# Kernel tuning notes

Measured on AMD Instinct MI355X. Metric: run time of the kernel, lower is better.

## Reference

```python
import jax, jax.numpy as jnp
import numpy as np

N, E = 50000, 800000
IN, H, OUT = 500, 128, 64


def _gcn_layer(x, src, dst, norm, W, b):
    # Linear transform first (PyG GCNConv applies lin before propagate)
    h = x @ W                                   # [N, F_out]
    msg = norm[:, None] * h[src]                # [E', F_out] gather
    out = jax.ops.segment_sum(msg, dst, num_segments=N)  # scatter-add
    return out + b


def setup_inputs() -> dict:
    key = jax.random.key(0)
    k = jax.random.split(key, 6)
    x = jax.random.normal(k[0], (N, IN), jnp.float32)
    edge_index = jax.random.randint(k[1], (2, E), 0, N, dtype=jnp.int32)
    # Glorot-style init like PyG GCNConv
    W1 = jax.random.normal(k[2], (IN, H), jnp.float32) * (1.0 / np.sqrt(IN))
    b1 = jnp.zeros((H,), jnp.float32)
    W2 = jax.random.normal(k[3], (H, OUT), jnp.float32) * (1.0 / np.sqrt(H))
    b2 = jnp.zeros((OUT,), jnp.float32)
    return {"x": x, "edge_index": edge_index, "W1": W1, "b1": b1, "W2": W2, "b2": b2}


def reference(x, edge_index, W1, b1, W2, b2):
    # Add self loops (PyG GCNConv default add_self_loops=True)
    loops = jnp.arange(N, dtype=edge_index.dtype)
    src = jnp.concatenate([edge_index[0], loops])
    dst = jnp.concatenate([edge_index[1], loops])
    # Symmetric degree normalization: deg computed on targets (col)
    deg = jax.ops.segment_sum(jnp.ones_like(src, dtype=x.dtype), dst, num_segments=N)
    dis = jnp.where(deg > 0, jax.lax.rsqrt(jnp.maximum(deg, 1.0)), 0.0)
    norm = dis[src] * dis[dst]                  # [E+N]
    h = jax.nn.relu(_gcn_layer(x, src, dst, norm, W1, b1))
    return _gcn_layer(h, src, dst, norm, W2, b2)
```

## Files before the change

kernel.cpp:

```cpp
#include <hip/hip_runtime.h>
#include <hip/hip_bf16.h>


typedef __attribute__((ext_vector_type(4))) float f32x4;
typedef __attribute__((ext_vector_type(8))) short short8;

static __device__ __forceinline__ unsigned short f2bf(float f) {
    unsigned int u = __float_as_uint(f);
    u += 0x7FFF + ((u >> 16) & 1);
    return (unsigned short)(u >> 16);
}
static __device__ __forceinline__ float bf2f(unsigned short h) {
    return __uint_as_float(((unsigned int)h) << 16);
}

static __device__ __forceinline__ void glds16(const void* g, void* l) {
    __builtin_amdgcn_global_load_lds(
        (const __attribute__((address_space(1))) void*)g,
        (__attribute__((address_space(3))) void*)l, 16, 0, 0);
}

__global__ void prep_deg(const float* __restrict__ W1, const float* __restrict__ W2,
                         unsigned short* __restrict__ I1, unsigned short* __restrict__ I2,
                         const int* __restrict__ dst, int* __restrict__ deg, int E) {
    const int bid = blockIdx.x;
    if (bid < 72) {
        int idx = bid * 256 + threadIdx.x;
        const int total1 = 16 * 1024;
        if (idx < total1) {
            int kt = idx >> 10, pl = (idx >> 9) & 1, slot = (idx >> 7) & 3, col = idx & 127;
            int k0 = kt * 32 + slot * 8;
#pragma unroll
            for (int j = 0; j < 8; j++) {
                int k = k0 + j;
                float v = (k < 500) ? W1[(size_t)k * 128 + col] : 0.f;
                unsigned short h = f2bf(v);
                I1[(size_t)idx * 8 + j] = pl ? f2bf(v - bf2f(h)) : h;
            }
        } else {
            int i2 = idx - total1;
            if (i2 < 2048) {
                int kt = i2 >> 9, pl = (i2 >> 8) & 1, slot = (i2 >> 6) & 3, col = i2 & 63;
                int k0 = kt * 32 + slot * 8;
#pragma unroll
                for (int j = 0; j < 8; j++) {
                    float v = W2[(size_t)(k0 + j) * 64 + col];
                    unsigned short h = f2bf(v);
                    I2[(size_t)i2 * 8 + j] = pl ? f2bf(v - bf2f(h)) : h;
                }
            }
        }
    } else {
        int e = (bid - 72) * 256 + threadIdx.x;
        if (e < E) atomicAdd(&deg[dst[e]], 1);
    }
}

__global__ void scan_part(const int* __restrict__ deg, int* __restrict__ bsum, int N) {
    int tid = threadIdx.x, lane = tid & 63, wid = tid >> 6;
    int i = blockIdx.x * 256 + tid;
    int v = (i < N) ? deg[i] : 0;
#pragma unroll
    for (int off = 1; off < 64; off <<= 1) v += __shfl_xor(v, off, 64);
    __shared__ int ws[4];
    if (lane == 0) ws[wid] = v;
    __syncthreads();
    if (tid == 0) bsum[blockIdx.x] = ws[0] + ws[1] + ws[2] + ws[3];
}

__global__ __launch_bounds__(1024) void scan_top(const int* __restrict__ bsum, int nb,
                                                 int* __restrict__ boff, int* __restrict__ rp, int N) {
    __shared__ int wsum[16];
    int tid = threadIdx.x, lane = tid & 63, wid = tid >> 6;
    int v = (tid < nb) ? bsum[tid] : 0;
    int x = v;
#pragma unroll
    for (int off = 1; off < 64; off <<= 1) {
        int t = __shfl_up(x, off, 64);
        if (lane >= off) x += t;
    }
    if (lane == 63) wsum[wid] = x;
    __syncthreads();
    if (tid < 16) {
        int y = wsum[tid];
#pragma unroll
        for (int off = 1; off < 16; off <<= 1) {
            int t = __shfl_up(y, off, 16);
            if (tid >= off) y += t;
        }
        wsum[tid] = y;
    }
    __syncthreads();
    int base = wid ? wsum[wid - 1] : 0;
    if (tid < nb) boff[tid] = base + x - v;
    if (tid == 0) rp[N] = wsum[15];
}

__global__ void scan_final(int* __restrict__ deg, const int* __restrict__ boff,
                           int* __restrict__ rp, int* __restrict__ cursor, int N) {
    int tid = threadIdx.x, lane = tid & 63, wid = tid >> 6;
    int i = blockIdx.x * 256 + tid;
    int v = (i < N) ? deg[i] : 0;
    int x = v;
#pragma unroll
    for (int off = 1; off < 64; off <<= 1) {
        int t = __shfl_up(x, off, 64);
        if (lane >= off) x += t;
    }
    __shared__ int wsum[4];
    if (lane == 63) wsum[wid] = x;
    __syncthreads();
    int base = boff[blockIdx.x];
    for (int ww = 0; ww < wid; ww++) base += wsum[ww];
    int ex = base + x - v;
    if (i < N) {
        rp[i] = ex;
        cursor[i] = ex;
        ((float*)deg)[i] = rsqrtf((float)(v + 1));
    }
}

template<int BN, int KT, int KFULL, bool ABF16>
__device__ __forceinline__ void gemm_body(
    int bid, unsigned char* sm,
    const void* __restrict__ Av, const unsigned char* __restrict__ Wimg,
    unsigned short* __restrict__ C, int M, int K) {
    constexpr int AELT = ABF16 ? 2 : 4;
    constexpr int ABYTES = 64 * 32 * AELT;
    constexpr int BBYTES = BN * 128;
    constexpr int STEP = ABYTES + BBYTES;
    constexpr int AINST = ABYTES / 1024;
    constexpr int BINST = BBYTES / 1024;
    constexpr int IPW = (AINST + BINST) / 4;
    constexpr int BIPW = BINST / 4;
    constexpr int NF = BN / 16;
    constexpr int AKC = 16 / AELT;

    const int tid = threadIdx.x, lane = tid & 63, w = tid >> 6;
    const int lrow = lane & 15, lq = lane >> 4;
    const int bm = bid * 64;

    f32x4 acc[NF] = {};

    float pr[8];
    if constexpr (!ABF16 && KFULL < KT) {
        const float* A = (const float*)Av;
        const int prow = tid >> 2, pk = (tid & 3) * 8;
        const int grow = bm + prow;
#pragma unroll
        for (int j = 0; j < 8; j++) {
            int k = KFULL * 32 + pk + j;
            pr[j] = (grow < M && k < K) ? A[(size_t)grow * K + k] : 0.f;
        }
    }

    auto STAGE = [&](int kt, int buf) {
        unsigned char* base = sm + buf * STEP;
#pragma unroll
        for (int j = 0; j < IPW; j++) {
            int g = w * IPW + j;
            if (g < AINST) {
                int srow = bm + lane; if (srow >= M) srow = M - 1;
                if constexpr (ABF16)
                    glds16((const unsigned short*)Av + (size_t)srow * K + kt * 32 + g * AKC,
                           base + g * 1024);
                else
                    glds16((const float*)Av + (size_t)srow * K + kt * 32 + g * AKC,
                           base + g * 1024);
            } else {
                int b = g - AINST;
                glds16(Wimg + (size_t)kt * BBYTES + (size_t)b * 1024 + lane * 16,
                       base + ABYTES + b * 1024);
            }
        }
    };
    auto STAGE_B = [&](int kt, int buf) {
        unsigned char* base = sm + buf * STEP;
#pragma unroll
        for (int j = 0; j < BIPW; j++) {
            int b = w * BIPW + j;
            glds16(Wimg + (size_t)kt * BBYTES + (size_t)b * 1024 + lane * 16,
                   base + ABYTES + b * 1024);
        }
    };
    auto REGWRITE = [&](int buf) {
        if constexpr (!ABF16) {
            const int prow = tid >> 2, pk = (tid & 3) * 8;
            unsigned char* base = sm + buf * STEP;
            int s0 = pk >> 2;
            *(float4*)(base + s0 * 1024 + prow * 16) = make_float4(pr[0], pr[1], pr[2], pr[3]);
            *(float4*)(base + (s0 + 1) * 1024 + prow * 16) = make_float4(pr[4], pr[5], pr[6], pr[7]);
        }
    };
    auto COMPUTE = [&](int buf) {
        const unsigned char* base = sm + buf * STEP;
        short8 ah, al;
        if constexpr (ABF16) {
            int r = w * 16 + lrow;
            ah = *(const short8*)(base + lq * 1024 + r * 16);
        } else {
            int r = w * 16 + lrow;
            float4 f0 = *(const float4*)(base + (lq * 2) * 1024 + r * 16);
            float4 f1 = *(const float4*)(base + (lq * 2 + 1) * 1024 + r * 16);
            float fv[8] = {f0.x, f0.y, f0.z, f0.w, f1.x, f1.y, f1.z, f1.w};
#pragma unroll
            for (int e = 0; e < 8; e++) {
                unsigned short hu = f2bf(fv[e]);
                ah[e] = (short)hu;
                al[e] = (short)f2bf(fv[e] - bf2f(hu));
            }
        }
        short8 bh[NF], bl[NF];
#pragma unroll
        for (int n = 0; n < NF; n++) {
            int c = n * 16 + lrow;
            bh[n] = *(const short8*)(base + ABYTES + lq * (BN * 16) + c * 16);
            bl[n] = *(const short8*)(base + ABYTES + BBYTES / 2 + lq * (BN * 16) + c * 16);
        }
#pragma unroll
        for (int n = 0; n < NF; n++) {
            acc[n] = __builtin_amdgcn_mfma_f32_16x16x32_bf16(ah, bh[n], acc[n], 0, 0, 0);
            if constexpr (!ABF16)
                acc[n] = __builtin_amdgcn_mfma_f32_16x16x32_bf16(al, bh[n], acc[n], 0, 0, 0);
            acc[n] = __builtin_amdgcn_mfma_f32_16x16x32_bf16(ah, bl[n], acc[n], 0, 0, 0);
        }
    };

    STAGE(0, 0);
    __syncthreads();
    int cur = 0;
    for (int kt = 0; kt < KT; kt++) {
        if (kt + 1 < KT) {
            if constexpr (!ABF16 && KFULL < KT) {
                if (kt + 1 == KFULL) { STAGE_B(kt + 1, cur ^ 1); REGWRITE(cur ^ 1); }
                else STAGE(kt + 1, cur ^ 1);
            } else {
                STAGE(kt + 1, cur ^ 1);
            }
        }
        COMPUTE(cur);
        __syncthreads();
        cur ^= 1;
    }

#pragma unroll
    for (int n = 0; n < NF; n++)
#pragma unroll
        for (int q = 0; q < 4; q++) {
            int row = bm + w * 16 + (lane >> 4) * 4 + q;
            int col = n * 16 + (lane & 15);
            if (row < M) C[(size_t)row * BN + col] = f2bf(acc[n][q]);
        }
}

template<int BN, int KT>
__global__ __launch_bounds__(256) void gemm_glds_bf(
    const unsigned short* __restrict__ A, const unsigned char* __restrict__ Wimg,
    unsigned short* __restrict__ C, int M, int K) {
    __shared__ unsigned char sm[2 * (4096 + BN * 128)];
    gemm_body<BN, KT, KT, true>(blockIdx.x, sm, A, Wimg, C, M, K);
}

template<int BN, int KT, int KFULL>
__global__ __launch_bounds__(256) void fat_gemm_csr(
    const float* __restrict__ A, const unsigned char* __restrict__ Wimg,
    unsigned short* __restrict__ C, int M, int K,
    const int* __restrict__ src, const int* __restrict__ dst,
    int* __restrict__ cursor, int* __restrict__ csr_src, int E,
    int ngemm, int ncsr) {
    __shared__ unsigned char sm[2 * (8192 + BN * 128)];
    const int bid = blockIdx.x;
    const int stripe = bid / 5, pos = bid % 5;
    if (pos == 0) {
        if (stripe < ngemm)
            gemm_body<BN, KT, KFULL, false>(stripe, sm, A, Wimg, C, M, K);
    } else {
        int c = stripe * 4 + pos - 1;
        if (c < ncsr) {
            int e = c * 256 + threadIdx.x;
            if (e < E) {
                int p = atomicAdd(&cursor[dst[e]], 1);
                csr_src[p] = src[e];
            }
        }
    }
}

__global__ __launch_bounds__(256) void gather128(
    const int* __restrict__ rp, const int* __restrict__ csr,
    const float* __restrict__ dis, const unsigned short* __restrict__ h,
    const float* __restrict__ bias, unsigned short* __restrict__ out, int Nn) {
    int n = (blockIdx.x * 256 + threadIdx.x) >> 6;
    int lane = threadIdx.x & 63;
    if (n >= Nn) return;
    const int hh = lane >> 5;
    const int l = lane & 31;
    int beg = rp[n], end = rp[n + 1];
    float4 a0 = {0,0,0,0}, a1 = {0,0,0,0}, a2 = {0,0,0,0}, a3 = {0,0,0,0};
    auto P = [&](int e, float4& a) {
        int s = csr[e];
        float w = dis[s];
        ushort4 v = *(const ushort4*)&h[(size_t)s * 128 + l * 4];
        a.x = fmaf(w, bf2f(v.x), a.x); a.y = fmaf(w, bf2f(v.y), a.y);
        a.z = fmaf(w, bf2f(v.z), a.z); a.w = fmaf(w, bf2f(v.w), a.w);
    };
    int j = beg + hh;
    for (; j + 6 < end; j += 8) { P(j, a0); P(j + 2, a1); P(j + 4, a2); P(j + 6, a3); }
    for (; j < end; j += 2) P(j, a0);
    float4 acc;
    acc.x = (a0.x + a1.x) + (a2.x + a3.x);
    acc.y = (a0.y + a1.y) + (a2.y + a3.y);
    acc.z = (a0.z + a1.z) + (a2.z + a3.z);
    acc.w = (a0.w + a1.w) + (a2.w + a3.w);
    acc.x += __shfl_xor(acc.x, 32);
    acc.y += __shfl_xor(acc.y, 32);
    acc.z += __shfl_xor(acc.z, 32);
    acc.w += __shfl_xor(acc.w, 32);
    float dn = dis[n];
    ushort4 hv = *(const ushort4*)&h[(size_t)n * 128 + l * 4];
    float4 b4 = *(const float4*)&bias[l * 4];
    if (hh == 0) {
        ushort4 o;
        o.x = f2bf(fmaxf(dn * (acc.x + dn * bf2f(hv.x)) + b4.x, 0.f));
        o.y = f2bf(fmaxf(dn * (acc.y + dn * bf2f(hv.y)) + b4.y, 0.f));
        o.z = f2bf(fmaxf(dn * (acc.z + dn * bf2f(hv.z)) + b4.z, 0.f));
        o.w = f2bf(fmaxf(dn * (acc.w + dn * bf2f(hv.w)) + b4.w, 0.f));
        *(ushort4*)&out[(size_t)n * 128 + l * 4] = o;
    }
}

__global__ __launch_bounds__(256) void gather64(
    const int* __restrict__ rp, const int* __restrict__ csr,
    const float* __restrict__ dis, const unsigned short* __restrict__ h,
    const float* __restrict__ bias, float* __restrict__ out, int Nn) {
    int n = (blockIdx.x * 256 + threadIdx.x) >> 6;
    int lane = threadIdx.x & 63;
    if (n >= Nn) return;
    const int q = lane >> 4;
    const int l = lane & 15;
    int beg = rp[n], end = rp[n + 1];
    float4 a0 = {0,0,0,0}, a1 = {0,0,0,0};
    auto P = [&](int e, float4& a) {
        int s = csr[e];
        float w = dis[s];
        ushort4 v = *(const ushort4*)&h[(size_t)s * 64 + l * 4];
        a.x = fmaf(w, bf2f(v.x), a.x); a.y = fmaf(w, bf2f(v.y), a.y);
        a.z = fmaf(w, bf2f(v.z), a.z); a.w = fmaf(w, bf2f(v.w), a.w);
    };
    int j = beg + q;
    for (; j + 4 < end; j += 8) { P(j, a0); P(j + 4, a1); }
    for (; j < end; j += 4) P(j, a0);
    float4 acc;
    acc.x = a0.x + a1.x; acc.y = a0.y + a1.y;
    acc.z = a0.z + a1.z; acc.w = a0.w + a1.w;
    acc.x += __shfl_xor(acc.x, 16); acc.x += __shfl_xor(acc.x, 32);
    acc.y += __shfl_xor(acc.y, 16); acc.y += __shfl_xor(acc.y, 32);
    acc.z += __shfl_xor(acc.z, 16); acc.z += __shfl_xor(acc.z, 32);
    acc.w += __shfl_xor(acc.w, 16); acc.w += __shfl_xor(acc.w, 32);
    float dn = dis[n];
    ushort4 hv = *(const ushort4*)&h[(size_t)n * 64 + l * 4];
    float4 b4 = *(const float4*)&bias[l * 4];
    float4 o;
    o.x = dn * (acc.x + dn * bf2f(hv.x)) + b4.x;
    o.y = dn * (acc.y + dn * bf2f(hv.y)) + b4.y;
    o.z = dn * (acc.z + dn * bf2f(hv.z)) + b4.z;
    o.w = dn * (acc.w + dn * bf2f(hv.w)) + b4.w;
    if (q == 0) *(float4*)&out[(size_t)n * 64 + l * 4] = o;
}

extern "C" void kernel_launch(void* const* d_in, const int* in_sizes, int n_in,
                              void* d_out, int out_size, void* d_ws, size_t ws_size,
                              hipStream_t stream) {
    const float* x  = (const float*)d_in[0];
    const int*   ei = (const int*)d_in[1];
    const float* W1 = (const float*)d_in[2];
    const float* b1 = (const float*)d_in[3];
    const float* W2 = (const float*)d_in[4];
    const float* b2 = (const float*)d_in[5];

    const int IN = 500, H = 128, OUT = 64;
    const int Nn = in_sizes[0] / IN;
    const int E  = in_sizes[1] / 2;
    const int* src  = ei;
    const int* dstp = ei + E;

    const int Npad = ((Nn + 63) / 64) * 64;
    const int nb   = (Nn + 255) / 256;
    const int ngemm = (Nn + 63) / 64;
    const int ncsr  = (E + 255) / 256;

    int*   degdis  = (int*)d_ws;
    int*   rp      = degdis + Npad;
    int*   bsum    = rp + Npad + 64;
    int*   boff    = bsum + 1024;
    int*   cursor  = boff + 1024;
    int*   csr_src = cursor + Npad;
    unsigned short* I1 = (unsigned short*)(csr_src + ((E + 63) / 64) * 64);
    unsigned short* I2 = I1 + 16 * 8192;
    unsigned short* h1u = I2 + 4 * 4096;
    unsigned short* agg1u = h1u + (size_t)Npad * H;
    unsigned short* h2u = h1u;
    float* dis     = (float*)degdis;
    float* out     = (float*)d_out;

    hipMemsetAsync(degdis, 0, (size_t)Nn * sizeof(int), stream);
    prep_deg<<<72 + ncsr, 256, 0, stream>>>(W1, W2, I1, I2, dstp, degdis, E);
    scan_part<<<nb, 256, 0, stream>>>(degdis, bsum, Nn);
    scan_top<<<1, 1024, 0, stream>>>(bsum, nb, boff, rp, Nn);
    scan_final<<<nb, 256, 0, stream>>>(degdis, boff, rp, cursor, Nn);

    fat_gemm_csr<128, 16, 15><<<ngemm * 5, 256, 0, stream>>>(
        x, (const unsigned char*)I1, h1u, Nn, IN,
        src, dstp, cursor, csr_src, E, ngemm, ncsr);

    gather128<<<(Nn + 3) / 4, 256, 0, stream>>>(rp, csr_src, dis, h1u, b1, agg1u, Nn);

    gemm_glds_bf<64, 4><<<ngemm, 256, 0, stream>>>(
        agg1u, (const unsigned char*)I2, h2u, Nn, H);
    gather64<<<(Nn + 3) / 4, 256, 0, stream>>>(rp, csr_src, dis, h2u, b2, out, Nn);
}
```

Measured before the change: 184.3 us.

## Shrink first-layer GEMM tile to 32 rows with 2x2 wave grid

The fused GEMM+CSR-build kernel now uses a 32-row M tile, with the four waves arranged as 2x2 (16 rows by 64 columns each) instead of four 16-row stripes over all 128 columns. This doubles the number of GEMM blocks for more parallelism across CUs. The interleave ratio changes from one GEMM block per four CSR blocks to one per two. The A-tile LDS layout and register prefetch are reworked to match. Each block still loads the full weight slice, so weight traffic per output row doubles, and the second-layer GEMM is split into its own standalone kernel.

```diff
diff --git a/kernel.cpp b/kernel.cpp
--- a/kernel.cpp
+++ b/kernel.cpp
@@ -120,36 +120,29 @@
     }
 }
 
-template<int BN, int KT, int KFULL, bool ABF16>
-__device__ __forceinline__ void gemm_body(
+template<int KT, int KFULL>
+__device__ __forceinline__ void gemm32_body(
     int bid, unsigned char* sm,
-    const void* __restrict__ Av, const unsigned char* __restrict__ Wimg,
+    const float* __restrict__ A, const unsigned char* __restrict__ Wimg,
     unsigned short* __restrict__ C, int M, int K) {
-    constexpr int AELT = ABF16 ? 2 : 4;
-    constexpr int ABYTES = 64 * 32 * AELT;
-    constexpr int BBYTES = BN * 128;
-    constexpr int STEP = ABYTES + BBYTES;
-    constexpr int AINST = ABYTES / 1024;
-    constexpr int BINST = BBYTES / 1024;
-    constexpr int IPW = (AINST + BINST) / 4;
-    constexpr int BIPW = BINST / 4;
-    constexpr int NF = BN / 16;
-    constexpr int AKC = 16 / AELT;
+    constexpr int ABYTES = 4096, BBYTES = 16384, STEP = ABYTES + BBYTES;
+    constexpr int NF = 4;
 
     const int tid = threadIdx.x, lane = tid & 63, w = tid >> 6;
     const int lrow = lane & 15, lq = lane >> 4;
-    const int bm = bid * 64;
+    const int wrow = (w >> 1) * 16;
+    const int wcol = (w & 1) * 64;
+    const int bm = bid * 32;
 
     f32x4 acc[NF] = {};
 
-    float pr[8];
-    if constexpr (!ABF16 && KFULL < KT) {
-        const float* A = (const float*)Av;
-        const int prow = tid >> 2, pk = (tid & 3) * 8;
+    float pr[4];
+    {
+        const int prow = tid >> 3, pkq = tid & 7;
         const int grow = bm + prow;
 #pragma unroll
-        for (int j = 0; j < 8; j++) {
-            int k = KFULL * 32 + pk + j;
+        for (int j = 0; j < 4; j++) {
+            int k = KFULL * 32 + pkq * 4 + j;
             pr[j] = (grow < M && k < K) ? A[(size_t)grow * K + k] : 0.f;
         }
     }
@@ -157,18 +150,15 @@
     auto STAGE = [&](int kt, int buf) {
         unsigned char* base = sm + buf * STEP;
 #pragma unroll
-        for (int j = 0; j < IPW; j++) {
-            int g = w * IPW + j;
-            if (g < AINST) {
-                int srow = bm + lane; if (srow >= M) srow = M - 1;
-                if constexpr (ABF16)
-                    glds16((const unsigned short*)Av + (size_t)srow * K + kt * 32 + g * AKC,
-                           base + g * 1024);
-                else
-                    glds16((const float*)Av + (size_t)srow * K + kt * 32 + g * AKC,
-                           base + g * 1024);
+        for (int j = 0; j < 5; j++) {
+            int g = w * 5 + j;
+            if (g < 4) {
+                int row = lane >> 1;
+                int srow = bm + row; if (srow >= M) srow = M - 1;
+                int kq = (lane & 1) + g * 2;
+                glds16(A + (size_t)srow * K + kt * 32 + kq * 4, base + g * 1024);
             } else {
-                int b = g - AINST;
+                int b = g - 4;
                 glds16(Wimg + (size_t)kt * BBYTES + (size_t)b * 1024 + lane * 16,
                        base + ABYTES + b * 1024);
             }
@@ -177,31 +167,25 @@
     auto STAGE_B = [&](int kt, int buf) {
         unsigned char* base = sm + buf * STEP;
 #pragma unroll
-        for (int j = 0; j < BIPW; j++) {
-            int b = w * BIPW + j;
+        for (int j = 0; j < 4; j++) {
+            int b = w * 4 + j;
             glds16(Wimg + (size_t)kt * BBYTES + (size_t)b * 1024 + lane * 16,
                    base + ABYTES + b * 1024);
         }
     };
     auto REGWRITE = [&](int buf) {
-        if constexpr (!ABF16) {
-            const int prow = tid >> 2, pk = (tid & 3) * 8;
-            unsigned char* base = sm + buf * STEP;
-            int s0 = pk >> 2;
-            *(float4*)(base + s0 * 1024 + prow * 16) = make_float4(pr[0], pr[1], pr[2], pr[3]);
-            *(float4*)(base + (s0 + 1) * 1024 + prow * 16) = make_float4(pr[4], pr[5], pr[6], pr[7]);
-        }
+        const int prow = tid >> 3, pkq = tid & 7;
+        unsigned char* base = sm + buf * STEP;
+        *(float4*)(base + (pkq >> 1) * 1024 + (prow * 2 + (pkq & 1)) * 16) =
+            make_float4(pr[0], pr[1], pr[2], pr[3]);
     };
     auto COMPUTE = [&](int buf) {
         const unsigned char* base = sm + buf * STEP;
         short8 ah, al;
-        if constexpr (ABF16) {
-            int r = w * 16 + lrow;
-            ah = *(const short8*)(base + lq * 1024 + r * 16);
-        } else {
-            int r = w * 16 + lrow;
-            float4 f0 = *(const float4*)(base + (lq * 2) * 1024 + r * 16);
-            float4 f1 = *(const float4*)(base + (lq * 2 + 1) * 1024 + r * 16);
+        {
+            int r = wrow + lrow;
+            float4 f0 = *(const float4*)(base + lq * 1024 + r * 32);
+            float4 f1 = *(const float4*)(base + lq * 1024 + r * 32 + 16);
             float fv[8] = {f0.x, f0.y, f0.z, f0.w, f1.x, f1.y, f1.z, f1.w};
 #pragma unroll
             for (int e = 0; e < 8; e++) {
@@ -213,15 +197,14 @@
         short8 bh[NF], bl[NF];
 #pragma unroll
         for (int n = 0; n < NF; n++) {
-            int c = n * 16 + lrow;
-            bh[n] = *(const short8*)(base + ABYTES + lq * (BN * 16) + c * 16);
-            bl[n] = *(const short8*)(base + ABYTES + BBYTES / 2 + lq * (BN * 16) + c * 16);
+            int c = wcol + n * 16 + lrow;
+            bh[n] = *(const short8*)(base + ABYTES + lq * 2048 + c * 16);
+            bl[n] = *(const short8*)(base + ABYTES + 8192 + lq * 2048 + c * 16);
         }
 #pragma unroll
         for (int n = 0; n < NF; n++) {
             acc[n] = __builtin_amdgcn_mfma_f32_16x16x32_bf16(ah, bh[n], acc[n], 0, 0, 0);
-            if constexpr (!ABF16)
-                acc[n] = __builtin_amdgcn_mfma_f32_16x16x32_bf16(al, bh[n], acc[n], 0, 0, 0);
+            acc[n] = __builtin_amdgcn_mfma_f32_16x16x32_bf16(al, bh[n], acc[n], 0, 0, 0);
             acc[n] = __builtin_amdgcn_mfma_f32_16x16x32_bf16(ah, bl[n], acc[n], 0, 0, 0);
         }
     };
@@ -231,12 +214,8 @@
     int cur = 0;
     for (int kt = 0; kt < KT; kt++) {
         if (kt + 1 < KT) {
-            if constexpr (!ABF16 && KFULL < KT) {
-                if (kt + 1 == KFULL) { STAGE_B(kt + 1, cur ^ 1); REGWRITE(cur ^ 1); }
-                else STAGE(kt + 1, cur ^ 1);
-            } else {
-                STAGE(kt + 1, cur ^ 1);
-            }
+            if (kt + 1 == KFULL) { STAGE_B(kt + 1, cur ^ 1); REGWRITE(cur ^ 1); }
+            else STAGE(kt + 1, cur ^ 1);
         }
         COMPUTE(cur);
         __syncthreads();
@@ -247,35 +226,27 @@
     for (int n = 0; n < NF; n++)
 #pragma unroll
         for (int q = 0; q < 4; q++) {
-            int row = bm + w * 16 + (lane >> 4) * 4 + q;
-            int col = n * 16 + (lane & 15);
-            if (row < M) C[(size_t)row * BN + col] = f2bf(acc[n][q]);
-        }
-}
-
-template<int BN, int KT>
-__global__ __launch_bounds__(256) void gemm_glds_bf(
-    const unsigned short* __restrict__ A, const unsigned char* __restrict__ Wimg,
-    unsigned short* __restrict__ C, int M, int K) {
-    __shared__ unsigned char sm[2 * (4096 + BN * 128)];
-    gemm_body<BN, KT, KT, true>(blockIdx.x, sm, A, Wimg, C, M, K);
-}
-
-template<int BN, int KT, int KFULL>
+            int row = bm + wrow + (lane >> 4) * 4 + q;
+            int col = wcol + n * 16 + (lane & 15);
+            if (row < M) C[(size_t)row * 128 + col] = f2bf(acc[n][q]);
+        }
+}
+
+template<int KT, int KFULL>
 __global__ __launch_bounds__(256) void fat_gemm_csr(
     const float* __restrict__ A, const unsigned char* __restrict__ Wimg,
     unsigned short* __restrict__ C, int M, int K,
     const int* __restrict__ src, const int* __restrict__ dst,
     int* __restrict__ cursor, int* __restrict__ csr_src, int E,
     int ngemm, int ncsr) {
-    __shared__ unsigned char sm[2 * (8192 + BN * 128)];
+    __shared__ unsigned char sm[2 * 20480];
     const int bid = blockIdx.x;
-    const int stripe = bid / 5, pos = bid % 5;
+    const int stripe = bid / 3, pos = bid % 3;
     if (pos == 0) {
         if (stripe < ngemm)
-            gemm_body<BN, KT, KFULL, false>(stripe, sm, A, Wimg, C, M, K);
+            gemm32_body<KT, KFULL>(stripe, sm, A, Wimg, C, M, K);
     } else {
-        int c = stripe * 4 + pos - 1;
+        int c = stripe * 2 + pos - 1;
         if (c < ncsr) {
             int e = c * 256 + threadIdx.x;
             if (e < E) {
@@ -284,6 +255,82 @@
             }
         }
     }
+}
+
+template<int BN, int KT>
+__global__ __launch_bounds__(256) void gemm_glds_bf(
+    const unsigned short* __restrict__ A, const unsigned char* __restrict__ Wimg,
+    unsigned short* __restrict__ C, int M, int K) {
+    constexpr int ABYTES = 64 * 32 * 2;
+    constexpr int BBYTES = BN * 128;
+    constexpr int STEP = ABYTES + BBYTES;
+    constexpr int AINST = ABYTES / 1024;
+    constexpr int BINST = BBYTES / 1024;
+    constexpr int IPW = (AINST + BINST) / 4;
+    constexpr int NF = BN / 16;
+
+    __shared__ unsigned char sm[2 * STEP];
+
+    const int tid = threadIdx.x, lane = tid & 63, w = tid >> 6;
+    const int lrow = lane & 15, lq = lane >> 4;
+    const int bm = blockIdx.x * 64;
+
+    f32x4 acc[NF] = {};
+
+    auto STAGE = [&](int kt, int buf) {
+        unsigned char* base = sm + buf * STEP;
+#pragma unroll
+        for (int j = 0; j < IPW; j++) {
+            int g = w * IPW + j;
+            if (g < AINST) {
+                int srow = bm + lane; if (srow >= M) srow = M - 1;
+                glds16(A + (size_t)srow * K + kt * 32 + g * 8, base + g * 1024);
+            } else {
+                int b = g - AINST;
+                glds16(Wimg + (size_t)kt * BBYTES + (size_t)b * 1024 + lane * 16,
+                       base + ABYTES + b * 1024);
+            }
+        }
+    };
+    auto COMPUTE = [&](int buf) {
+        const unsigned char* base = sm + buf * STEP;
+        short8 ah;
+        {
+            int r = w * 16 + lrow;
+            ah = *(const short8*)(base + lq * 1024 + r * 16);
+        }
+        short8 bh[NF], bl[NF];
+#pragma unroll
+        for (int n = 0; n < NF; n++) {
+            int c = n * 16 + lrow;
+            bh[n] = *(const short8*)(base + ABYTES + lq * (BN * 16) + c * 16);
+            bl[n] = *(const short8*)(base + ABYTES + BBYTES / 2 + lq * (BN * 16) + c * 16);
+        }
+#pragma unroll
+        for (int n = 0; n < NF; n++) {
+            acc[n] = __builtin_amdgcn_mfma_f32_16x16x32_bf16(ah, bh[n], acc[n], 0, 0, 0);
+            acc[n] = __builtin_amdgcn_mfma_f32_16x16x32_bf16(ah, bl[n], acc[n], 0, 0, 0);
+        }
+    };
+
+    STAGE(0, 0);
+    __syncthreads();
+    int cur = 0;
+    for (int kt = 0; kt < KT; kt++) {
+        if (kt + 1 < KT) STAGE(kt + 1, cur ^ 1);
+        COMPUTE(cur);
+        __syncthreads();
+        cur ^= 1;
+    }
+
+#pragma unroll
+    for (int n = 0; n < NF; n++)
+#pragma unroll
+        for (int q = 0; q < 4; q++) {
+            int row = bm + w * 16 + (lane >> 4) * 4 + q;
+            int col = n * 16 + (lane & 15);
+            if (row < M) C[(size_t)row * BN + col] = f2bf(acc[n][q]);
+        }
 }
 
 __global__ __launch_bounds__(256) void gather128(
@@ -386,7 +433,8 @@
 
     const int Npad = ((Nn + 63) / 64) * 64;
     const int nb   = (Nn + 255) / 256;
-    const int ngemm = (Nn + 63) / 64;
+    const int ngemm1 = (Nn + 31) / 32;
+    const int ngemm2 = (Nn + 63) / 64;
     const int ncsr  = (E + 255) / 256;
 
     int*   degdis  = (int*)d_ws;
@@ -409,13 +457,13 @@
     scan_top<<<1, 1024, 0, stream>>>(bsum, nb, boff, rp, Nn);
     scan_final<<<nb, 256, 0, stream>>>(degdis, boff, rp, cursor, Nn);
 
-    fat_gemm_csr<128, 16, 15><<<ngemm * 5, 256, 0, stream>>>(
+    fat_gemm_csr<16, 15><<<ngemm1 * 3, 256, 0, stream>>>(
         x, (const unsigned char*)I1, h1u, Nn, IN,
-        src, dstp, cursor, csr_src, E, ngemm, ncsr);
+        src, dstp, cursor, csr_src, E, ngemm1, ncsr);
 
     gather128<<<(Nn + 3) / 4, 256, 0, stream>>>(rp, csr_src, dis, h1u, b1, agg1u, Nn);
 
-    gemm_glds_bf<64, 4><<<ngemm, 256, 0, stream>>>(
+    gemm_glds_bf<64, 4><<<ngemm2, 256, 0, stream>>>(
         agg1u, (const unsigned char*)I2, h2u, Nn, H);
     gather64<<<(Nn + 3) / 4, 256, 0, stream>>>(rp, csr_src, dis, h2u, b2, out, Nn);
 }
```

Result: no change. 181.7 us (-1.4%).
